# Kernel tuning notes

Hardware: AMD Instinct MI355X
Metric: run time of the kernel (lower is better)

## Reference

```python
import jax, jax.numpy as jnp
import numpy as np


def setup_inputs() -> dict:
    key = jax.random.key(0)
    ks = jax.random.split(key, 8)
    B, C, N = 4, 256, 4096
    C4 = C // 4
    x = jax.random.normal(ks[0], (B, C, N), dtype=jnp.float32)
    # conv1x1 weights == channel-mixing matrices [out_ch, in_ch]
    Wq = jax.random.normal(ks[1], (C4, C), dtype=jnp.float32) * (1.0 / np.sqrt(C))
    bq = jax.random.normal(ks[2], (C4,), dtype=jnp.float32) * 0.02
    Wk = jax.random.normal(ks[3], (C4, C), dtype=jnp.float32) * (1.0 / np.sqrt(C))
    bk = jax.random.normal(ks[4], (C4,), dtype=jnp.float32) * 0.02
    Wv = jax.random.normal(ks[5], (C, C), dtype=jnp.float32) * (1.0 / np.sqrt(C))
    bv = jax.random.normal(ks[6], (C,), dtype=jnp.float32) * 0.02
    # nn.Parameter(torch.zeros(1)) -> but use nonzero so grads flow through attn path
    gamma = jax.random.normal(ks[7], (1,), dtype=jnp.float32) * 0.1
    return {"x": x, "Wq": Wq, "bq": bq, "Wk": Wk, "bk": bk,
            "Wv": Wv, "bv": bv, "gamma": gamma}


def reference(x, Wq, bq, Wk, bk, Wv, bv, gamma):
    # x: [B, C, N]; conv1x1 == matmul over channel dim
    q = jnp.einsum('oc,bcn->bon', Wq, x) + bq[None, :, None]   # [B, C/4, N]
    k = jnp.einsum('oc,bcn->bon', Wk, x) + bk[None, :, None]   # [B, C/4, N]
    v = jnp.einsum('oc,bcn->bon', Wv, x) + bv[None, :, None]   # [B, C,   N]
    # energy[b, i, j] = <q[:, i], k[:, j]>  (unscaled)
    energy = jnp.einsum('bdi,bdj->bij', q, k)                  # [B, N, N]
    attn = jax.nn.softmax(energy, axis=-1)                     # softmax over j
    # out[b, c, i] = sum_j v[b, c, j] * attn[b, i, j]
    out = jnp.einsum('bcj,bij->bci', v, attn)                  # [B, C, N]
    return gamma[0] * out + x
```

## Files before the change

kernel.cpp:

```cpp
#include <hip/hip_runtime.h>

#define NPTS 4096
#define CDIM 256
#define C4DIM 64

typedef __bf16 bf16x8 __attribute__((ext_vector_type(8)));
typedef float  f32x4  __attribute__((ext_vector_type(4)));

__device__ __forceinline__ void async_cp16(const void* g, void* l) {
    __builtin_amdgcn_global_load_lds(
        (const __attribute__((address_space(1))) void*)g,
        (__attribute__((address_space(3))) void*)l, 16, 0, 0);
}

__global__ __launch_bounds__(256) void wprep_kernel(
    const float* __restrict__ Wq, const float* __restrict__ Wk,
    const float* __restrict__ Wv, __bf16* __restrict__ wsz)
{
    int idx = blockIdx.x * 256 + threadIdx.x;
    int row = idx >> 6;
    int l   = idx & 63;
    const float* src;
    if (row < 64)       src = Wq + (size_t)row * CDIM;
    else if (row < 128) src = Wk + (size_t)(row - 64) * CDIM;
    else                src = Wv + (size_t)(row - 128) * CDIM;
    float4 f = *(const float4*)&src[l * 4];
    int g  = l >> 1;
    int gp = g ^ (row & 7);
    union { __bf16 h[4]; uint2 u; } pk;
    pk.h[0] = (__bf16)f.x; pk.h[1] = (__bf16)f.y;
    pk.h[2] = (__bf16)f.z; pk.h[3] = (__bf16)f.w;
    *(uint2*)&wsz[(size_t)row * CDIM + gp * 8 + (l & 1) * 4] = pk.u;
}

__global__ __launch_bounds__(256, 2) void proj_kernel(
    const float* __restrict__ x,
    const float* __restrict__ bq, const float* __restrict__ bk,
    const float* __restrict__ bv, const __bf16* __restrict__ wsz,
    __bf16* __restrict__ qT, __bf16* __restrict__ kT, __bf16* __restrict__ vo)
{
    __shared__ __align__(16) unsigned char sm[65536];
    auto Xs = (float (*)[33])sm;

    const int t    = threadIdx.x;
    const int w    = t >> 6;
    const int lane = t & 63;
    const int quad = lane >> 4;
    const int l16  = lane & 15;
    const int nq   = w >> 1;
    const int th   = w & 1;

    const int n0 = blockIdx.x * 32;
    const int b  = blockIdx.y;

    #pragma unroll
    for (int s = 0; s < 8; s++) {
        int lin = t + 256 * s;
        int c = lin >> 3, n4 = (lin & 7) * 4;
        *(float4*)&Xs[c][n4] =
            *(const float4*)&x[((size_t)b * CDIM + c) * NPTS + n0 + n4];
    }
    __syncthreads();

    bf16x8 af[8];
    #pragma unroll
    for (int kc = 0; kc < 8; kc++) {
        union { __bf16 h8[8]; bf16x8 v; } pk;
        #pragma unroll
        for (int u = 0; u < 8; u++)
            pk.h8[u] = (__bf16)Xs[kc * 32 + quad * 8 + u][16 * nq + l16];
        af[kc] = pk.v;
    }
    __syncthreads();

    const int lhalf = lane >> 5;
    const int rlow  = (2 * w + lhalf) & 7;
    const int slane = ((lane & 31) ^ rlow) * 8;

    #pragma unroll
    for (int s = 0; s < 8; s++)
        async_cp16(wsz + (size_t)(8 * s + 2 * w + lhalf) * CDIM + slane,
                   sm + (s * 4 + w) * 1024);

    f32x4 acc[6][2];
    #pragma unroll
    for (int ot = 0; ot < 6; ot++) {
        acc[ot][0] = (f32x4)(0.f);
        acc[ot][1] = (f32x4)(0.f);
    }

    #pragma unroll
    for (int ot = 0; ot < 6; ot++) {
        __syncthreads();
        if (ot < 5) {
            #pragma unroll
            for (int s = 0; s < 8; s++)
                async_cp16(wsz + (size_t)((ot + 1) * 64 + 8 * s + 2 * w + lhalf) * CDIM + slane,
                           sm + ((ot + 1) & 1) * 32768 + (s * 4 + w) * 1024);
        }
        const unsigned char* Wp = sm + (ot & 1) * 32768;
        #pragma unroll
        for (int kc = 0; kc < 8; kc++) {
            bf16x8 bw[2];
            #pragma unroll
            for (int tcl = 0; tcl < 2; tcl++)
                bw[tcl] = *(const bf16x8*)(Wp + (16 * (2 * th + tcl) + l16) * 512
                                              + (((kc * 4 + quad) ^ (l16 & 7)) << 4));
            #pragma unroll
            for (int tcl = 0; tcl < 2; tcl++)
                acc[ot][tcl] = __builtin_amdgcn_mfma_f32_16x16x32_bf16(
                    af[kc], bw[tcl], acc[ot][tcl], 0, 0, 0);
        }
    }

    {
        auto OT = (float (*)[68])sm;
        #pragma unroll
        for (int ot = 0; ot < 2; ot++) {
            __syncthreads();
            const float* bias = ot ? bk : bq;
            #pragma unroll
            for (int tcl = 0; tcl < 2; tcl++) {
                float bs = bias[16 * (2 * th + tcl) + l16];
                #pragma unroll
                for (int r4 = 0; r4 < 4; r4++)
                    OT[16 * nq + 4 * quad + r4][16 * (2 * th + tcl) + l16] =
                        acc[ot][tcl][r4] + bs;
            }
            __syncthreads();
            __bf16* outp = (ot == 0 ? qT : kT) + (size_t)b * NPTS * C4DIM;
            int n = t >> 3, op = (t & 7) * 8;
            f32x4 o0 = *(const f32x4*)&OT[n][op];
            f32x4 o1 = *(const f32x4*)&OT[n][op + 4];
            union { __bf16 h[8]; uint4 u; } pk;
            #pragma unroll
            for (int u2 = 0; u2 < 4; u2++) {
                pk.h[u2]     = (__bf16)o0[u2];
                pk.h[u2 + 4] = (__bf16)o1[u2];
            }
            *(uint4*)&outp[(size_t)(n0 + n) * C4DIM + op] = pk.u;
        }
    }
    {
        auto OTv = (float (*)[36])sm;
        #pragma unroll
        for (int ot = 2; ot < 6; ot++) {
            __syncthreads();
            #pragma unroll
            for (int tcl = 0; tcl < 2; tcl++) {
                float bs = bv[(ot - 2) * 64 + 16 * (2 * th + tcl) + l16];
                f32x4 v4 = acc[ot][tcl];
                v4[0] += bs; v4[1] += bs; v4[2] += bs; v4[3] += bs;
                *(f32x4*)&OTv[16 * (2 * th + tcl) + l16][16 * nq + 4 * quad] = v4;
            }
            __syncthreads();
            int cl = t >> 2, np = (t & 3) * 8;
            int ch = (ot - 2) * 64 + cl;
            f32x4 o0 = *(const f32x4*)&OTv[cl][np];
            f32x4 o1 = *(const f32x4*)&OTv[cl][np + 4];
            union { __bf16 h[8]; uint4 u; } pk;
            #pragma unroll
            for (int u2 = 0; u2 < 4; u2++) {
                pk.h[u2]     = (__bf16)o0[u2];
                pk.h[u2 + 4] = (__bf16)o1[u2];
            }
            *(uint4*)&vo[((size_t)b * CDIM + ch) * NPTS + n0 + np] = pk.u;
        }
    }
}

__global__ __launch_bounds__(256, 2) void attn_kernel(
    const __bf16* __restrict__ qT, const __bf16* __restrict__ kT,
    const __bf16* __restrict__ vin, const float* __restrict__ xin,
    const float* __restrict__ gptr, float* __restrict__ out)
{
    __shared__ __align__(16) unsigned char sm[41984];
    unsigned char* Vb = sm;
    auto Ps  = (__bf16 (*)[72])(sm + 32768);
    auto OTa = (float (*)[68])sm;
    float* Lp = (float*)(sm + 34816);

    const int t    = threadIdx.x;
    const int w    = t >> 6;
    const int lane = t & 63;
    const int quad = lane >> 4;
    const int l16  = lane & 15;
    const int r    = w >> 1;
    const int jh   = w & 1;

    const int b  = blockIdx.z;
    const int i0 = blockIdx.x * 64;
    const int c0 = blockIdx.y * 128;

    const __bf16* qb = qT  + (size_t)b * NPTS * C4DIM;
    const __bf16* kb = kT  + (size_t)b * NPTS * C4DIM;
    const __bf16* vb = vin + (size_t)b * CDIM * NPTS;

    const int swz = (lane & 7) ^ ((lane >> 3) & 7);
    int voff[4];
    #pragma unroll
    for (int s = 0; s < 4; s++) {
        int row = (4 * w + s) * 8 + (lane >> 3);
        voff[s] = (c0 + row) * (NPTS * 2) + swz * 16;
    }

    bf16x8 aq[2][2];
    #pragma unroll
    for (int rt = 0; rt < 2; rt++)
        #pragma unroll
        for (int kc = 0; kc < 2; kc++)
            aq[rt][kc] = *(const bf16x8*)&qb[(size_t)(i0 + 32 * r + 16 * rt + l16) * C4DIM
                                             + kc * 32 + quad * 8];

    bf16x8 vone;
    #pragma unroll
    for (int u = 0; u < 8; u++) vone[u] = (__bf16)1.0f;

    f32x4 O[2][8], lacc[2];
    #pragma unroll
    for (int rt = 0; rt < 2; rt++) {
        lacc[rt] = (f32x4)(0.f);
        #pragma unroll
        for (int tc = 0; tc < 8; tc++) O[rt][tc] = (f32x4)(0.f);
    }

    bf16x8 kr0[2][2], kr1[2][2];
    #pragma unroll
    for (int kc = 0; kc < 2; kc++)
        #pragma unroll
        for (int ct = 0; ct < 2; ct++)
            kr0[kc][ct] = *(const bf16x8*)&kb[(size_t)(32 * jh + 16 * ct + l16) * C4DIM
                                              + kc * 32 + quad * 8];

    {
        const char* vbase = (const char*)vb;
        #pragma unroll
        for (int s = 0; s < 4; s++) async_cp16(vbase + voff[s], Vb + (4 * w + s) * 1024);
    }

    auto body = [&](int j0, const unsigned char* V, unsigned char* Vd,
                    bf16x8 (&kcur)[2][2], bf16x8 (&knext)[2][2]) {
        __syncthreads();

        const int jn = j0 + 64;
        if (jn < NPTS) {
            const char* vbase = (const char*)vb + (size_t)jn * 2;
            #pragma unroll
            for (int s = 0; s < 4; s++) async_cp16(vbase + voff[s], Vd + (4 * w + s) * 1024);
        }
        const int jk = jn & (NPTS - 1);
        #pragma unroll
        for (int kc = 0; kc < 2; kc++)
            #pragma unroll
            for (int ct = 0; ct < 2; ct++)
                knext[kc][ct] = *(const bf16x8*)&kb[(size_t)(jk + 32 * jh + 16 * ct + l16) * C4DIM
                                                    + kc * 32 + quad * 8];

        f32x4 S[2][2];
        #pragma unroll
        for (int rt = 0; rt < 2; rt++)
            #pragma unroll
            for (int ct = 0; ct < 2; ct++) S[rt][ct] = (f32x4)(0.f);
        #pragma unroll
        for (int kc = 0; kc < 2; kc++)
            #pragma unroll
            for (int rt = 0; rt < 2; rt++)
                #pragma unroll
                for (int ct = 0; ct < 2; ct++)
                    S[rt][ct] = __builtin_amdgcn_mfma_f32_16x16x32_bf16(
                        kcur[kc][ct], aq[rt][kc], S[rt][ct], 0, 0, 0);

        #pragma unroll
        for (int rt = 0; rt < 2; rt++)
            #pragma unroll
            for (int ct = 0; ct < 2; ct++) {
                union { __bf16 h[4]; uint2 u; } pk;
                #pragma unroll
                for (int r4 = 0; r4 < 4; r4++)
                    pk.h[r4] = (__bf16)__expf(S[rt][ct][r4] - 32.0f);
                *(uint2*)&Ps[32 * r + 16 * rt + l16][32 * jh + 16 * ct + 4 * quad] = pk.u;
            }

        bf16x8 ap[2];
        #pragma unroll
        for (int rt = 0; rt < 2; rt++)
            ap[rt] = *(const bf16x8*)((const char*)&Ps[32 * r + 16 * rt + l16][0]
                                      + jh * 64 + quad * 16);
        __builtin_amdgcn_s_setprio(1);
        #pragma unroll
        for (int tc = 0; tc < 8; tc++) {
            int row = 16 * tc + l16;
            int slot = (jh * 4 + quad) ^ (l16 & 7);
            bf16x8 bv2 = *(const bf16x8*)(V + row * 128 + slot * 16);
            #pragma unroll
            for (int rt = 0; rt < 2; rt++)
                O[rt][tc] = __builtin_amdgcn_mfma_f32_16x16x32_bf16(
                    ap[rt], bv2, O[rt][tc], 0, 0, 0);
        }
        #pragma unroll
        for (int rt = 0; rt < 2; rt++)
            lacc[rt] = __builtin_amdgcn_mfma_f32_16x16x32_bf16(ap[rt], vone, lacc[rt], 0, 0, 0);
        __builtin_amdgcn_s_setprio(0);
    };

    for (int jj = 0; jj < NPTS; jj += 128) {
        body(jj,      Vb,         Vb + 16384, kr0, kr1);
        body(jj + 64, Vb + 16384, Vb,         kr1, kr0);
    }

    __syncthreads();
    const float g = gptr[0];

    if (jh == 1) {
        float* dst = (float*)(sm + (size_t)(r * 64 + lane) * 272);
        #pragma unroll
        for (int rt = 0; rt < 2; rt++)
            #pragma unroll
            for (int tc = 0; tc < 8; tc++)
                *(f32x4*)(dst + (rt * 8 + tc) * 4) = O[rt][tc];
        if (l16 == 0) {
            #pragma unroll
            for (int rt = 0; rt < 2; rt++)
                #pragma unroll
                for (int r4 = 0; r4 < 4; r4++)
                    Lp[32 * r + 16 * rt + 4 * quad + r4] = lacc[rt][r4];
        }
    }
    __syncthreads();

    float inv[2][4];
    if (jh == 0) {
        const float* src = (const float*)(sm + (size_t)(r * 64 + lane) * 272);
        #pragma unroll
        for (int rt = 0; rt < 2; rt++)
            #pragma unroll
            for (int tc = 0; tc < 8; tc++)
                O[rt][tc] += *(const f32x4*)(src + (rt * 8 + tc) * 4);
        #pragma unroll
        for (int rt = 0; rt < 2; rt++)
            #pragma unroll
            for (int r4 = 0; r4 < 4; r4++) {
                float ls = lacc[rt][r4] + Lp[32 * r + 16 * rt + 4 * quad + r4];
                inv[rt][r4] = g / ls;
            }
    }
    __syncthreads();

    if (jh == 0) {
        #pragma unroll
        for (int rt = 0; rt < 2; rt++)
            #pragma unroll
            for (int tc = 0; tc < 8; tc++) {
                int c = 16 * tc + l16;
                float4 f;
                f.x = O[rt][tc][0] * inv[rt][0];
                f.y = O[rt][tc][1] * inv[rt][1];
                f.z = O[rt][tc][2] * inv[rt][2];
                f.w = O[rt][tc][3] * inv[rt][3];
                *(float4*)&OTa[c][32 * r + 16 * rt + 4 * quad] = f;
            }
    }
    __syncthreads();

    const float* xb = xin + (size_t)b * CDIM * NPTS;
    float*       ob = out + (size_t)b * CDIM * NPTS;
    #pragma unroll
    for (int s = 0; s < 8; s++) {
        int lin = t + 256 * s;
        int c = lin >> 4, col = (lin & 15) * 4;
        size_t gi = (size_t)(c0 + c) * NPTS + i0 + col;
        float4 ov = *(const float4*)&OTa[c][col];
        float4 xv = *(const float4*)&xb[gi];
        float4 rr;
        rr.x = ov.x + xv.x; rr.y = ov.y + xv.y;
        rr.z = ov.z + xv.z; rr.w = ov.w + xv.w;
        *(float4*)&ob[gi] = rr;
    }
}

extern "C" void kernel_launch(void* const* d_in, const int* in_sizes, int n_in,
                              void* d_out, int out_size, void* d_ws, size_t ws_size,
                              hipStream_t stream) {
    const float* x     = (const float*)d_in[0];
    const float* Wq    = (const float*)d_in[1];
    const float* bq    = (const float*)d_in[2];
    const float* Wk    = (const float*)d_in[3];
    const float* bk    = (const float*)d_in[4];
    const float* Wv    = (const float*)d_in[5];
    const float* bv    = (const float*)d_in[6];
    const float* gamma = (const float*)d_in[7];

    const int B = 4;
    __bf16* qT  = (__bf16*)d_ws;
    __bf16* kT  = qT + (size_t)B * NPTS * C4DIM;
    __bf16* v   = kT + (size_t)B * NPTS * C4DIM;
    __bf16* wsz = v  + (size_t)B * CDIM * NPTS;

    wprep_kernel<<<96, 256, 0, stream>>>(Wq, Wk, Wv, wsz);

    proj_kernel<<<dim3(NPTS/32, B), 256, 0, stream>>>(
        x, bq, bk, bv, wsz, qT, kT, v);

    attn_kernel<<<dim3(NPTS/64, CDIM/128, B), 256, 0, stream>>>(
        qT, kT, v, x, gamma, (float*)d_out);
}
```

Measured before the change: 176.8 us.

## Stage K tiles through LDS with async copies alongside V double buffer

K tiles are now loaded into a swizzled, double-buffered LDS region with async global-to-LDS copies, replacing per-lane register prefetch from global memory. The MFMA operand order is swapped, so P is written to LDS transposed as scalar bf16 stores. exp is rewritten as exp2 with a fused multiply-add. LDS use grows to about 57 KB per block, which could limit the two-blocks-per-CU target, and the scalar P stores may cause bank conflicts.

After: 163.4 us. -7.6%, faster.

```diff
diff --git a/kernel.cpp b/kernel.cpp
--- a/kernel.cpp
+++ b/kernel.cpp
@@ -174,9 +174,10 @@
     const __bf16* __restrict__ vin, const float* __restrict__ xin,
     const float* __restrict__ gptr, float* __restrict__ out)
 {
-    __shared__ __align__(16) unsigned char sm[41984];
-    unsigned char* Vb = sm;
-    auto Ps  = (__bf16 (*)[72])(sm + 32768);
+    __shared__ __align__(16) unsigned char sm[58368];
+    unsigned char* Kb = sm;
+    unsigned char* Vb = sm + 16384;
+    auto Ps  = (__bf16 (*)[72])(sm + 49152);
     auto OTa = (float (*)[68])sm;
     float* Lp = (float*)(sm + 34816);
 
@@ -197,7 +198,12 @@
     const __bf16* vb = vin + (size_t)b * CDIM * NPTS;
 
     const int swz = (lane & 7) ^ ((lane >> 3) & 7);
-    int voff[4];
+    int koff[2], voff[4];
+    #pragma unroll
+    for (int s = 0; s < 2; s++) {
+        int row = (2 * w + s) * 8 + (lane >> 3);
+        koff[s] = row * 128 + swz * 16;
+    }
     #pragma unroll
     for (int s = 0; s < 4; s++) {
         int row = (4 * w + s) * 8 + (lane >> 3);
@@ -224,37 +230,32 @@
         for (int tc = 0; tc < 8; tc++) O[rt][tc] = (f32x4)(0.f);
     }
 
-    bf16x8 kr0[2][2], kr1[2][2];
-    #pragma unroll
-    for (int kc = 0; kc < 2; kc++)
-        #pragma unroll
-        for (int ct = 0; ct < 2; ct++)
-            kr0[kc][ct] = *(const bf16x8*)&kb[(size_t)(32 * jh + 16 * ct + l16) * C4DIM
-                                              + kc * 32 + quad * 8];
-
     {
+        const char* kbase = (const char*)kb;
         const char* vbase = (const char*)vb;
         #pragma unroll
+        for (int s = 0; s < 2; s++) async_cp16(kbase + koff[s], Kb + (2 * w + s) * 1024);
+        #pragma unroll
         for (int s = 0; s < 4; s++) async_cp16(vbase + voff[s], Vb + (4 * w + s) * 1024);
     }
 
-    auto body = [&](int j0, const unsigned char* V, unsigned char* Vd,
-                    bf16x8 (&kcur)[2][2], bf16x8 (&knext)[2][2]) {
+    int p = 0;
+    for (int j0 = 0; j0 < NPTS; j0 += 64, p ^= 1) {
         __syncthreads();
 
-        const int jn = j0 + 64;
-        if (jn < NPTS) {
-            const char* vbase = (const char*)vb + (size_t)jn * 2;
+        if (j0 + 64 < NPTS) {
+            const char* kbase = (const char*)kb + (size_t)(j0 + 64) * (C4DIM * 2);
+            const char* vbase = (const char*)vb + (size_t)(j0 + 64) * 2;
+            unsigned char* Kd = Kb + (p ^ 1) * 8192;
+            unsigned char* Vd = Vb + (p ^ 1) * 16384;
+            #pragma unroll
+            for (int s = 0; s < 2; s++) async_cp16(kbase + koff[s], Kd + (2 * w + s) * 1024);
             #pragma unroll
             for (int s = 0; s < 4; s++) async_cp16(vbase + voff[s], Vd + (4 * w + s) * 1024);
         }
-        const int jk = jn & (NPTS - 1);
-        #pragma unroll
-        for (int kc = 0; kc < 2; kc++)
-            #pragma unroll
-            for (int ct = 0; ct < 2; ct++)
-                knext[kc][ct] = *(const bf16x8*)&kb[(size_t)(jk + 32 * jh + 16 * ct + l16) * C4DIM
-                                                    + kc * 32 + quad * 8];
+
+        const unsigned char* K = Kb + p * 8192;
+        const unsigned char* V = Vb + p * 16384;
 
         f32x4 S[2][2];
         #pragma unroll
@@ -262,24 +263,32 @@
             #pragma unroll
             for (int ct = 0; ct < 2; ct++) S[rt][ct] = (f32x4)(0.f);
         #pragma unroll
-        for (int kc = 0; kc < 2; kc++)
+        for (int kc = 0; kc < 2; kc++) {
+            bf16x8 bk2[2];
+            #pragma unroll
+            for (int ct = 0; ct < 2; ct++) {
+                int row = 32 * jh + 16 * ct + l16;
+                int slot = (kc * 4 + quad) ^ (l16 & 7);
+                bk2[ct] = *(const bf16x8*)(K + row * 128 + slot * 16);
+            }
             #pragma unroll
             for (int rt = 0; rt < 2; rt++)
                 #pragma unroll
                 for (int ct = 0; ct < 2; ct++)
                     S[rt][ct] = __builtin_amdgcn_mfma_f32_16x16x32_bf16(
-                        kcur[kc][ct], aq[rt][kc], S[rt][ct], 0, 0, 0);
-
-        #pragma unroll
-        for (int rt = 0; rt < 2; rt++)
-            #pragma unroll
-            for (int ct = 0; ct < 2; ct++) {
-                union { __bf16 h[4]; uint2 u; } pk;
+                        aq[rt][kc], bk2[ct], S[rt][ct], 0, 0, 0);
+        }
+
+        #pragma unroll
+        for (int rt = 0; rt < 2; rt++)
+            #pragma unroll
+            for (int ct = 0; ct < 2; ct++)
                 #pragma unroll
                 for (int r4 = 0; r4 < 4; r4++)
-                    pk.h[r4] = (__bf16)__expf(S[rt][ct][r4] - 32.0f);
-                *(uint2*)&Ps[32 * r + 16 * rt + l16][32 * jh + 16 * ct + 4 * quad] = pk.u;
-            }
+                    Ps[32 * r + 16 * rt + 4 * quad + r4][32 * jh + 16 * ct + l16] =
+                        (__bf16)__builtin_amdgcn_exp2f(
+                            __builtin_fmaf(S[rt][ct][r4], 1.44269504088896340736f,
+                                           -46.16624130844683f));
 
         bf16x8 ap[2];
         #pragma unroll
@@ -301,11 +310,6 @@
         for (int rt = 0; rt < 2; rt++)
             lacc[rt] = __builtin_amdgcn_mfma_f32_16x16x32_bf16(ap[rt], vone, lacc[rt], 0, 0, 0);
         __builtin_amdgcn_s_setprio(0);
-    };
-
-    for (int jj = 0; jj < NPTS; jj += 128) {
-        body(jj,      Vb,         Vb + 16384, kr0, kr1);
-        body(jj + 64, Vb + 16384, Vb,         kr1, kr0);
     }
 
     __syncthreads();
```

## Stream V directly into registers and drop LDS staging and per-iteration barriers

Applied to the files above, without the earlier changes.

The V tile is no longer staged through double-buffered LDS with async global-to-LDS copies. Each wave now loads its own V fragments from global memory into a register double buffer, alongside the K fragments. Because each wave only touches its own slice of the P tile, the per-iteration __syncthreads can be removed. The score MFMA operands are swapped, so P is written transposed with scalar bf16 stores, and exp is computed as exp2 of an fma. The trade-offs are more VGPRs, global loads that hit strided rows and are duplicated across waves and blocks, and possible LDS bank conflicts from the scalar P stores.

After: 267.2 us. 51.1% more time.

```diff
diff --git a/kernel.cpp b/kernel.cpp
--- a/kernel.cpp
+++ b/kernel.cpp
@@ -174,11 +174,8 @@
     const __bf16* __restrict__ vin, const float* __restrict__ xin,
     const float* __restrict__ gptr, float* __restrict__ out)
 {
-    __shared__ __align__(16) unsigned char sm[41984];
-    unsigned char* Vb = sm;
-    auto Ps  = (__bf16 (*)[72])(sm + 32768);
-    auto OTa = (float (*)[68])sm;
-    float* Lp = (float*)(sm + 34816);
+    __shared__ __align__(16) unsigned char sm[35072];
+    auto Ps  = (__bf16 (*)[72])sm;
 
     const int t    = threadIdx.x;
     const int w    = t >> 6;
@@ -196,14 +193,6 @@
     const __bf16* kb = kT  + (size_t)b * NPTS * C4DIM;
     const __bf16* vb = vin + (size_t)b * CDIM * NPTS;
 
-    const int swz = (lane & 7) ^ ((lane >> 3) & 7);
-    int voff[4];
-    #pragma unroll
-    for (int s = 0; s < 4; s++) {
-        int row = (4 * w + s) * 8 + (lane >> 3);
-        voff[s] = (c0 + row) * (NPTS * 2) + swz * 16;
-    }
-
     bf16x8 aq[2][2];
     #pragma unroll
     for (int rt = 0; rt < 2; rt++)
@@ -224,37 +213,30 @@
         for (int tc = 0; tc < 8; tc++) O[rt][tc] = (f32x4)(0.f);
     }
 
-    bf16x8 kr0[2][2], kr1[2][2];
-    #pragma unroll
-    for (int kc = 0; kc < 2; kc++)
-        #pragma unroll
-        for (int ct = 0; ct < 2; ct++)
-            kr0[kc][ct] = *(const bf16x8*)&kb[(size_t)(32 * jh + 16 * ct + l16) * C4DIM
-                                              + kc * 32 + quad * 8];
-
-    {
-        const char* vbase = (const char*)vb;
-        #pragma unroll
-        for (int s = 0; s < 4; s++) async_cp16(vbase + voff[s], Vb + (4 * w + s) * 1024);
-    }
-
-    auto body = [&](int j0, const unsigned char* V, unsigned char* Vd,
-                    bf16x8 (&kcur)[2][2], bf16x8 (&knext)[2][2]) {
-        __syncthreads();
-
-        const int jn = j0 + 64;
-        if (jn < NPTS) {
-            const char* vbase = (const char*)vb + (size_t)jn * 2;
-            #pragma unroll
-            for (int s = 0; s < 4; s++) async_cp16(vbase + voff[s], Vd + (4 * w + s) * 1024);
-        }
-        const int jk = jn & (NPTS - 1);
+    auto kload = [&](bf16x8 (&dst)[2][2], int j) {
         #pragma unroll
         for (int kc = 0; kc < 2; kc++)
             #pragma unroll
             for (int ct = 0; ct < 2; ct++)
-                knext[kc][ct] = *(const bf16x8*)&kb[(size_t)(jk + 32 * jh + 16 * ct + l16) * C4DIM
-                                                    + kc * 32 + quad * 8];
+                dst[kc][ct] = *(const bf16x8*)&kb[(size_t)(j + 32 * jh + 16 * ct + l16) * C4DIM
+                                                  + kc * 32 + quad * 8];
+    };
+    auto vload = [&](bf16x8 (&dst)[8], int j) {
+        #pragma unroll
+        for (int tc = 0; tc < 8; tc++)
+            dst[tc] = *(const bf16x8*)&vb[(size_t)(c0 + 16 * tc + l16) * NPTS
+                                          + j + 32 * jh + quad * 8];
+    };
+
+    bf16x8 kr0[2][2], kr1[2][2], vr0[8], vr1[8];
+    kload(kr0, 0);
+    vload(vr0, 0);
+
+    auto body = [&](int j0, bf16x8 (&kcur)[2][2], bf16x8 (&knext)[2][2],
+                    bf16x8 (&vcur)[8], bf16x8 (&vnext)[8]) {
+        const int jk = (j0 + 64) & (NPTS - 1);
+        kload(knext, jk);
+        vload(vnext, jk);
 
         f32x4 S[2][2];
         #pragma unroll
@@ -268,18 +250,18 @@
                 #pragma unroll
                 for (int ct = 0; ct < 2; ct++)
                     S[rt][ct] = __builtin_amdgcn_mfma_f32_16x16x32_bf16(
-                        kcur[kc][ct], aq[rt][kc], S[rt][ct], 0, 0, 0);
-
-        #pragma unroll
-        for (int rt = 0; rt < 2; rt++)
-            #pragma unroll
-            for (int ct = 0; ct < 2; ct++) {
-                union { __bf16 h[4]; uint2 u; } pk;
+                        aq[rt][kc], kcur[kc][ct], S[rt][ct], 0, 0, 0);
+
+        #pragma unroll
+        for (int rt = 0; rt < 2; rt++)
+            #pragma unroll
+            for (int ct = 0; ct < 2; ct++)
                 #pragma unroll
                 for (int r4 = 0; r4 < 4; r4++)
-                    pk.h[r4] = (__bf16)__expf(S[rt][ct][r4] - 32.0f);
-                *(uint2*)&Ps[32 * r + 16 * rt + l16][32 * jh + 16 * ct + 4 * quad] = pk.u;
-            }
+                    Ps[32 * r + 16 * rt + 4 * quad + r4][32 * jh + 16 * ct + l16] =
+                        (__bf16)__builtin_amdgcn_exp2f(
+                            __builtin_fmaf(S[rt][ct][r4], 1.44269504088896340736f,
+                                           -46.16624130844683f));
 
         bf16x8 ap[2];
         #pragma unroll
@@ -288,15 +270,11 @@
                                       + jh * 64 + quad * 16);
         __builtin_amdgcn_s_setprio(1);
         #pragma unroll
-        for (int tc = 0; tc < 8; tc++) {
-            int row = 16 * tc + l16;
-            int slot = (jh * 4 + quad) ^ (l16 & 7);
-            bf16x8 bv2 = *(const bf16x8*)(V + row * 128 + slot * 16);
+        for (int tc = 0; tc < 8; tc++)
             #pragma unroll
             for (int rt = 0; rt < 2; rt++)
                 O[rt][tc] = __builtin_amdgcn_mfma_f32_16x16x32_bf16(
-                    ap[rt], bv2, O[rt][tc], 0, 0, 0);
-        }
+                    ap[rt], vcur[tc], O[rt][tc], 0, 0, 0);
         #pragma unroll
         for (int rt = 0; rt < 2; rt++)
             lacc[rt] = __builtin_amdgcn_mfma_f32_16x16x32_bf16(ap[rt], vone, lacc[rt], 0, 0, 0);
@@ -304,12 +282,13 @@
     };
 
     for (int jj = 0; jj < NPTS; jj += 128) {
-        body(jj,      Vb,         Vb + 16384, kr0, kr1);
-        body(jj + 64, Vb + 16384, Vb,         kr1, kr0);
+        body(jj,      kr0, kr1, vr0, vr1);
+        body(jj + 64, kr1, kr0, vr1, vr0);
     }
 
     __syncthreads();
     const float g = gptr[0];
+    float* Lp = (float*)(sm + 34816);
 
     if (jh == 1) {
         float* dst = (float*)(sm + (size_t)(r * 64 + lane) * 272);
@@ -346,6 +325,7 @@
     }
     __syncthreads();
 
+    auto OTa = (float (*)[68])sm;
     if (jh == 0) {
         #pragma unroll
         for (int rt = 0; rt < 2; rt++)
```
